# Optimization experiments

Measured on AMD Instinct MI355X. Metric: run time of the kernel, lower is better.

## Reference

```python
import jax, jax.numpy as jnp
import numpy as np

N = 50000
E = 800000
F_IN = 2      # num_node_features
H = 2         # heads
C = 64        # embedding_size (per-head out channels)
HID = 128     # hidden_size (message dim)
B = 512       # number of messages
NEG_SLOPE = 0.2


def gatv2_conv(x, src, dst, edge_attr, Wl, bl, Wr, br, We, att, bias):
    # x: [N, F_IN]; src/dst: [E]; edge_attr: [E, 1]
    n = x.shape[0]
    xl = (x @ Wl + bl).reshape(n, H, C)   # source transform (lin_l)
    xr = (x @ Wr + br).reshape(n, H, C)   # target transform (lin_r)
    ea = (edge_attr @ We).reshape(-1, H, C)
    m = xl[src] + xr[dst] + ea                      # [E, H, C]
    e = jnp.where(m > 0, m, NEG_SLOPE * m)          # LeakyReLU
    score = jnp.einsum('ehc,hc->eh', e, att)        # [E, H]
    # scatter-softmax over incoming edges of each target node
    smax = jax.ops.segment_max(score, dst, num_segments=n)
    smax = jnp.where(jnp.isfinite(smax), smax, 0.0)
    ex = jnp.exp(score - smax[dst])
    denom = jax.ops.segment_sum(ex, dst, num_segments=n)
    alpha = ex / (denom[dst] + 1e-16)               # [E, H]
    out = jax.ops.segment_sum(xl[src] * alpha[:, :, None], dst, num_segments=n)
    return out.reshape(n, H * C) + bias


def setup_inputs() -> dict:
    key = jax.random.key(0)
    ks = jax.random.split(key, 20)
    s = 0.1
    inp = {
        'message': jax.random.normal(ks[0], (B, HID), jnp.float32),
        'x': jax.random.normal(ks[1], (N, F_IN), jnp.float32),
        'edge_index': jax.random.randint(ks[2], (2, E), 0, N, jnp.int32),
        'edge_attr': jax.random.normal(ks[3], (E, 1), jnp.float32),
    }
    def conv_params(base):
        return {
            'Wl': jax.random.normal(ks[base], (F_IN, H * C)) * s,
            'bl': jnp.zeros((H * C,), jnp.float32),
            'Wr': jax.random.normal(ks[base + 1], (F_IN, H * C)) * s,
            'br': jnp.zeros((H * C,), jnp.float32),
            'We': jax.random.normal(ks[base + 2], (1, H * C)) * s,
            'att': jax.random.normal(ks[base + 3], (H, C)) * s,
            'bias': jnp.zeros((H * C,), jnp.float32),
        }
    p1 = {k + '1': v for k, v in conv_params(4).items()}
    p2 = {k + '2': v for k, v in conv_params(8).items()}
    inp.update(p1)
    inp.update(p2)
    inp['Wfc'] = jax.random.normal(ks[12], (HID, H * C)) * s
    inp['bfc'] = jnp.zeros((H * C,), jnp.float32)
    return inp


def reference(message, x, edge_index, edge_attr,
              Wl1, bl1, Wr1, br1, We1, att1, bias1,
              Wl2, bl2, Wr2, br2, We2, att2, bias2,
              Wfc, bfc):
    src, dst = edge_index[0], edge_index[1]
    # conv1 output is computed but unused in the original forward (conv2 takes x again)
    h1 = jax.nn.relu(gatv2_conv(x, src, dst, edge_attr, Wl1, bl1, Wr1, br1, We1, att1, bias1))
    h = jax.nn.relu(gatv2_conv(x, src, dst, edge_attr, Wl2, bl2, Wr2, br2, We2, att2, bias2))
    msg = jnp.concatenate([message, message], axis=0)      # [2B, HID]
    msg_emb = msg @ Wfc + bfc                              # [2B, H*C]
    dot = h @ msg_emb.T                                    # [N, 2B]
    return jax.nn.softmax(dot, axis=0)
```

## Files before the change

kernel.cpp:

```cpp
#include <hip/hip_runtime.h>
#include <hip/hip_bf16.h>
#include <hip/hip_cooperative_groups.h>

namespace cg = cooperative_groups;

#define N_NODES 50000
#define N_EDGES 800000
#define GRID    512
#define BLK     256
#define STRIDE  (GRID*BLK)
#define CHUNK   98
#define NTILES  782
#define NB_SCAN 196

typedef __attribute__((ext_vector_type(8))) short short8;
typedef __attribute__((ext_vector_type(16))) float f32x16;

struct Params {
  const float* msg; const float* x; const int* ei; const float* ea;
  const float* Wl; const float* bl; const float* Wr; const float* br;
  const float* We; const float* att; const float* bias;
  const float* Wfc; const float* bfc;
  float4* rec; float* nodeF;
  __hip_bfloat16* me_hi; __hip_bfloat16* me_lo;
  int* cnt; float* colsum; int* offs; int* cursor; int* bsum;
  float* dout;
};

template<int PASS>
__device__ __forceinline__ void mfma_tile(const Params& P, int tile, char* SMEM)
{
  short8* Bt = (short8*)SMEM;
  float* colacc = (float*)(SMEM + 32768);
  float* xp     = (float*)(SMEM + 32768);
  float* rcol   = (float*)(SMEM + 50176);

  const int tid = threadIdx.x;
  const int l = tid & 63, w = tid >> 6;
  const int rt = w >> 1, ct = w & 1;
  const int lrow = l & 31, lhalf = l >> 5;
  const int m0 = tile * 64;
  const int row = m0 + rt * 32 + lrow;

  float c0a = 0.f, c0b = 0.f, c0d = 0.f, c1a = 0.f, c1b = 0.f, c1d = 0.f;
  bool live = row < N_NODES;
  if (live) {
    const float* nf = P.nodeF + (size_t)row * 8;
    float D0 = nf[0], A00 = nf[1], A10 = nf[2];
    float D1 = nf[3], A01 = nf[4], A11 = nf[5];
    float r0 = 1.0f / (D0 + 1e-16f), r1 = 1.0f / (D1 + 1e-16f);
    c0a = A00 * r0; c0b = A10 * r0; c0d = D0 * r0;
    c1a = A01 * r1; c1b = A11 * r1; c1d = D1 * r1;
  }
  short8 a_hi[8], a_lo[8];
  #pragma unroll
  for (int ks = 0; ks < 8; ++ks) {
    int k0 = ks * 16 + lhalf * 8;
    float ca = (ks < 4) ? c0a : c1a;
    float cbv = (ks < 4) ? c0b : c1b;
    float cd = (ks < 4) ? c0d : c1d;
    float wA[8], wB[8], wC[8], wD[8];
    *(float4*)&wA[0] = *(const float4*)(P.Wl + k0);
    *(float4*)&wA[4] = *(const float4*)(P.Wl + k0 + 4);
    *(float4*)&wB[0] = *(const float4*)(P.Wl + 128 + k0);
    *(float4*)&wB[4] = *(const float4*)(P.Wl + 128 + k0 + 4);
    *(float4*)&wC[0] = *(const float4*)(P.bl + k0);
    *(float4*)&wC[4] = *(const float4*)(P.bl + k0 + 4);
    *(float4*)&wD[0] = *(const float4*)(P.bias + k0);
    *(float4*)&wD[4] = *(const float4*)(P.bias + k0 + 4);
    short8 hi8, lo8;
    #pragma unroll
    for (int j = 0; j < 8; ++j) {
      float v = ca * wA[j] + cbv * wB[j] + cd * wC[j] + wD[j];
      v = (live && v > 0.f) ? v : 0.f;
      __hip_bfloat16 hb = __float2bfloat16(v);
      float rem = v - __bfloat162float(hb);
      __hip_bfloat16 lb = __float2bfloat16(rem);
      short hs, ls;
      __builtin_memcpy(&hs, &hb, 2);
      __builtin_memcpy(&ls, &lb, 2);
      hi8[j] = hs; lo8[j] = ls;
    }
    a_hi[ks] = hi8; a_lo[ks] = lo8;
  }

  for (int cb = 0; cb < 8; ++cb) {
    __syncthreads();
    #pragma unroll
    for (int q = 0; q < 8; ++q) {
      int lin = q * 256 + tid;
      int s = lin & 1023;
      int col = s >> 4, ku = s & 15;
      int slot = ku * 64 + (col ^ ku);
      size_t gb = ((size_t)(cb * 64 + col) << 7) + ku * 8;
      if (lin < 1024) Bt[slot] = *(const short8*)(P.me_hi + gb);
      else            Bt[1024 + slot] = *(const short8*)(P.me_lo + gb);
    }
    __syncthreads();

    f32x16 acc = {0.f};
    #pragma unroll
    for (int ks = 0; ks < 8; ++ks) {
      int ku = ks * 2 + lhalf;
      int colB = ct * 32 + lrow;
      int slot = ku * 64 + (colB ^ ku);
      short8 bh = Bt[slot];
      short8 blo = Bt[1024 + slot];
      acc = __builtin_amdgcn_mfma_f32_32x32x16_bf16(a_hi[ks], bh, acc, 0, 0, 0);
      acc = __builtin_amdgcn_mfma_f32_32x32x16_bf16(a_lo[ks], bh, acc, 0, 0, 0);
      acc = __builtin_amdgcn_mfma_f32_32x32x16_bf16(a_hi[ks], blo, acc, 0, 0, 0);
    }

    if (PASS == 0) {
      float csum = 0.f;
      #pragma unroll
      for (int i = 0; i < 16; ++i) {
        int grow = m0 + rt * 32 + (i & 3) + 8 * (i >> 2) + 4 * lhalf;
        csum += (grow < N_NODES) ? __expf(acc[i]) : 0.f;
      }
      csum += __shfl_xor(csum, 32);
      if (l < 32) colacc[rt * 512 + cb * 64 + ct * 32 + l] += csum;
    } else {
      #pragma unroll
      for (int i = 0; i < 16; ++i) {
        int rl = rt * 32 + (i & 3) + 8 * (i >> 2) + 4 * lhalf;
        xp[rl * 68 + ct * 32 + lrow] = __expf(acc[i]);
      }
      __syncthreads();
      #pragma unroll
      for (int q = 0; q < 4; ++q) {
        int fid = q * 256 + tid;
        int rl = fid >> 4, c4 = fid & 15;
        int grow = m0 + rl;
        float4 v = *(float4*)&xp[rl * 68 + c4 * 4];
        float4 s = *(const float4*)&rcol[cb * 64 + c4 * 4];
        v.x *= s.x; v.y *= s.y; v.z *= s.z; v.w *= s.w;
        if (grow < N_NODES) {
          *(float4*)&P.dout[(size_t)grow * 1024 + cb * 64 + c4 * 4] = v;
          *(float4*)&P.dout[(size_t)grow * 1024 + 512 + cb * 64 + c4 * 4] = v;
        }
      }
    }
  }
}

__global__ __launch_bounds__(BLK, 2) void k_all(Params P)
{
  cg::grid_group gg = cg::this_grid();
  __shared__ __align__(16) char SMEM[52224];
  const int b = blockIdx.x, t = threadIdx.x;

  if (b < 256) {
    float* mrow = (float*)SMEM;
    int r = 2 * b + (t >> 7);
    int col = t & 127;
    mrow[t] = P.msg[r * 128 + col];
    __syncthreads();
    int base = (t >> 7) * 128;
    float acc = P.bfc[col];
    #pragma unroll 8
    for (int k = 0; k < 128; ++k) acc = fmaf(mrow[base + k], P.Wfc[k * 128 + col], acc);
    __hip_bfloat16 hi = __float2bfloat16(acc);
    P.me_hi[r * 128 + col] = hi;
    P.me_lo[r * 128 + col] = __float2bfloat16(acc - __bfloat162float(hi));
  } else if (b < 454) {
    int i = (b - 256) * 256 + t;
    if (i < N_NODES + 512) P.cnt[i] = 0;
  }
  gg.sync();

  for (int e = b * BLK + t; e < N_EDGES; e += STRIDE)
    atomicAdd(&P.cnt[P.ei[N_EDGES + e]], 1);
  gg.sync();

  {
    int* sh = (int*)SMEM;
    int base = b * CHUNK;
    if (t < 128) sh[t] = 0;
    __syncthreads();
    int v = 0;
    if (t < CHUNK && base + t < N_NODES) { v = P.cnt[base + t]; sh[t] = v; }
    __syncthreads();
    #pragma unroll
    for (int off = 1; off < 128; off <<= 1) {
      int u = (t < 128 && t >= off) ? sh[t - off] : 0;
      __syncthreads();
      if (t < 128) sh[t] += u;
      __syncthreads();
    }
    if (t < CHUNK && base + t < N_NODES) P.offs[base + t] = sh[t] - v;
    if (t == 0) P.bsum[b] = sh[127];
  }
  gg.sync();

  {
    int* eb = (int*)SMEM;
    int* s3 = eb + 512;
    int x0 = P.bsum[2 * t], x1 = P.bsum[2 * t + 1];
    s3[t] = x0 + x1;
    __syncthreads();
    #pragma unroll
    for (int off = 1; off < 256; off <<= 1) {
      int u = (t >= off) ? s3[t - off] : 0;
      __syncthreads();
      s3[t] += u;
      __syncthreads();
    }
    int p = t ? s3[t - 1] : 0;
    eb[2 * t] = p; eb[2 * t + 1] = p + x0;
    __syncthreads();
    int pb = eb[b];
    int base = b * CHUNK;
    if (t < CHUNK && base + t < N_NODES) {
      int o = P.offs[base + t] + pb;
      P.offs[base + t] = o;
      P.cursor[base + t] = o;
    }
    if (b == 0 && t == 0) P.offs[N_NODES] = N_EDGES;
  }
  gg.sync();

  for (int e = b * BLK + t; e < N_EDGES; e += STRIDE) {
    int s = P.ei[e], d = P.ei[N_EDGES + e];
    float x0s = P.x[2*s], x1s = P.x[2*s+1];
    float x0d = P.x[2*d], x1d = P.x[2*d+1];
    float av = P.ea[e];
    float s0 = 0.f, s1 = 0.f;
    #pragma unroll 8
    for (int k = 0; k < 64; ++k) {
      float m = P.bl[k] + P.br[k];
      m = fmaf(x0s, P.Wl[k], m);
      m = fmaf(x1s, P.Wl[128+k], m);
      m = fmaf(x0d, P.Wr[k], m);
      m = fmaf(x1d, P.Wr[128+k], m);
      m = fmaf(av, P.We[k], m);
      float lk = m > 0.f ? m : 0.2f * m;
      s0 = fmaf(lk, P.att[k], s0);
    }
    #pragma unroll 8
    for (int k = 64; k < 128; ++k) {
      float m = P.bl[k] + P.br[k];
      m = fmaf(x0s, P.Wl[k], m);
      m = fmaf(x1s, P.Wl[128+k], m);
      m = fmaf(x0d, P.Wr[k], m);
      m = fmaf(x1d, P.Wr[128+k], m);
      m = fmaf(av, P.We[k], m);
      float lk = m > 0.f ? m : 0.2f * m;
      s1 = fmaf(lk, P.att[k], s1);
    }
    int pos = atomicAdd(&P.cursor[d], 1);
    P.rec[pos] = make_float4(s0, s1, x0s, x1s);
  }
  gg.sync();

  {
    int n = b * BLK + t;
    if (n < N_NODES) {
      int a = P.offs[n], bb = P.offs[n + 1];
      float D0 = 0.f, A00 = 0.f, A10 = 0.f;
      float D1 = 0.f, A01 = 0.f, A11 = 0.f;
      for (int i = a; i < bb; ++i) {
        float4 r = P.rec[i];
        float e0 = __expf(r.x);
        float e1 = __expf(r.y);
        D0 += e0; A00 += e0 * r.z; A10 += e0 * r.w;
        D1 += e1; A01 += e1 * r.z; A11 += e1 * r.w;
      }
      float* nf = P.nodeF + (size_t)n * 8;
      nf[0] = D0; nf[1] = A00; nf[2] = A10;
      nf[3] = D1; nf[4] = A01; nf[5] = A11;
    }
  }
  gg.sync();

  {
    float* colacc = (float*)(SMEM + 32768);
    #pragma unroll
    for (int q = 0; q < 4; ++q) colacc[q * 256 + t] = 0.f;
    __syncthreads();
    for (int tile = b; tile < NTILES; tile += GRID)
      mfma_tile<0>(P, tile, SMEM);
    __syncthreads();
    atomicAdd(&P.colsum[t], colacc[t] + colacc[512 + t]);
    atomicAdd(&P.colsum[t + 256], colacc[256 + t] + colacc[768 + t]);
  }
  gg.sync();

  {
    float* rcol = (float*)(SMEM + 50176);
    rcol[t] = 1.0f / P.colsum[t];
    rcol[t + 256] = 1.0f / P.colsum[t + 256];
    __syncthreads();
    for (int tile = b; tile < NTILES; tile += GRID)
      mfma_tile<1>(P, tile, SMEM);
  }
}

__global__ __launch_bounds__(256) void k_zero(int* __restrict__ buf)
{
  int i = blockIdx.x * 256 + threadIdx.x;
  if (i < N_NODES + 512) buf[i] = 0;
}

__global__ __launch_bounds__(256) void k_hist(
    const int* __restrict__ ei, int* __restrict__ cnt)
{
  int e = blockIdx.x * 256 + threadIdx.x;
  if (e >= N_EDGES) return;
  atomicAdd(&cnt[ei[N_EDGES + e]], 1);
}

__global__ __launch_bounds__(256) void k_scan1(
    const int* __restrict__ cnt, int* __restrict__ offs, int* __restrict__ bsum)
{
  __shared__ int sh[256];
  int b = blockIdx.x, t = threadIdx.x;
  int i = b * 256 + t;
  int v = (i < N_NODES) ? cnt[i] : 0;
  sh[t] = v;
  __syncthreads();
  #pragma unroll
  for (int off = 1; off < 256; off <<= 1) {
    int u = (t >= off) ? sh[t - off] : 0;
    __syncthreads();
    sh[t] += u;
    __syncthreads();
  }
  if (i < N_NODES) offs[i] = sh[t] - v;
  if (t == 255) bsum[b] = sh[255];
}

__global__ __launch_bounds__(256) void k_scan2(int* __restrict__ bsum)
{
  __shared__ int sh[256];
  int t = threadIdx.x;
  int v = (t < NB_SCAN) ? bsum[t] : 0;
  sh[t] = v;
  __syncthreads();
  #pragma unroll
  for (int off = 1; off < 256; off <<= 1) {
    int u = (t >= off) ? sh[t - off] : 0;
    __syncthreads();
    sh[t] += u;
    __syncthreads();
  }
  if (t < NB_SCAN) bsum[t] = sh[t] - v;
}

__global__ __launch_bounds__(256) void k_scan3(
    int* __restrict__ offs, const int* __restrict__ bsum, int* __restrict__ cursor)
{
  int b = blockIdx.x, t = threadIdx.x;
  int i = b * 256 + t;
  if (i < N_NODES) {
    int o = offs[i] + bsum[b];
    offs[i] = o;
    cursor[i] = o;
  }
  if (b == 0 && t == 0) offs[N_NODES] = N_EDGES;
}

__global__ __launch_bounds__(256) void k_scatter(Params P)
{
  int e = blockIdx.x * 256 + threadIdx.x;
  if (e >= N_EDGES) return;
  int s = P.ei[e], d = P.ei[N_EDGES + e];
  float x0s = P.x[2*s], x1s = P.x[2*s+1];
  float x0d = P.x[2*d], x1d = P.x[2*d+1];
  float av = P.ea[e];
  float s0 = 0.f, s1 = 0.f;
  #pragma unroll 8
  for (int k = 0; k < 64; ++k) {
    float m = P.bl[k] + P.br[k];
    m = fmaf(x0s, P.Wl[k], m);
    m = fmaf(x1s, P.Wl[128+k], m);
    m = fmaf(x0d, P.Wr[k], m);
    m = fmaf(x1d, P.Wr[128+k], m);
    m = fmaf(av, P.We[k], m);
    float lk = m > 0.f ? m : 0.2f * m;
    s0 = fmaf(lk, P.att[k], s0);
  }
  #pragma unroll 8
  for (int k = 64; k < 128; ++k) {
    float m = P.bl[k] + P.br[k];
    m = fmaf(x0s, P.Wl[k], m);
    m = fmaf(x1s, P.Wl[128+k], m);
    m = fmaf(x0d, P.Wr[k], m);
    m = fmaf(x1d, P.Wr[128+k], m);
    m = fmaf(av, P.We[k], m);
    float lk = m > 0.f ? m : 0.2f * m;
    s1 = fmaf(lk, P.att[k], s1);
  }
  int pos = atomicAdd(&P.cursor[d], 1);
  P.rec[pos] = make_float4(s0, s1, x0s, x1s);
}

__global__ __launch_bounds__(256) void k_gather(Params P)
{
  int n = blockIdx.x * 256 + threadIdx.x;
  if (n >= N_NODES) return;
  int a = P.offs[n], b = P.offs[n + 1];
  float D0 = 0.f, A00 = 0.f, A10 = 0.f;
  float D1 = 0.f, A01 = 0.f, A11 = 0.f;
  for (int i = a; i < b; ++i) {
    float4 r = P.rec[i];
    float e0 = __expf(r.x);
    float e1 = __expf(r.y);
    D0 += e0; A00 += e0 * r.z; A10 += e0 * r.w;
    D1 += e1; A01 += e1 * r.z; A11 += e1 * r.w;
  }
  float* nf = P.nodeF + (size_t)n * 8;
  nf[0] = D0; nf[1] = A00; nf[2] = A10;
  nf[3] = D1; nf[4] = A01; nf[5] = A11;
}

__global__ __launch_bounds__(128) void k_fc(Params P)
{
  int j = blockIdx.x, k = threadIdx.x;
  __shared__ float mrow[128];
  mrow[k] = P.msg[j*128 + k];
  __syncthreads();
  float acc = P.bfc[k];
  #pragma unroll 8
  for (int t = 0; t < 128; ++t) acc = fmaf(mrow[t], P.Wfc[t*128 + k], acc);
  __hip_bfloat16 hi = __float2bfloat16(acc);
  P.me_hi[j*128 + k] = hi;
  P.me_lo[j*128 + k] = __float2bfloat16(acc - __bfloat162float(hi));
}

template<int PASS>
__global__ __launch_bounds__(256, 2) void k_mfma(Params P)
{
  __shared__ __align__(16) char SMEM[52224];
  int tid = threadIdx.x;
  if (PASS == 0) {
    float* colacc = (float*)(SMEM + 32768);
    #pragma unroll
    for (int q = 0; q < 4; ++q) colacc[q * 256 + tid] = 0.f;
    __syncthreads();
    mfma_tile<0>(P, blockIdx.x, SMEM);
    __syncthreads();
    atomicAdd(&P.colsum[tid], colacc[tid] + colacc[512 + tid]);
    atomicAdd(&P.colsum[tid + 256], colacc[256 + tid] + colacc[768 + tid]);
  } else {
    float* rcol = (float*)(SMEM + 50176);
    rcol[tid] = 1.0f / P.colsum[tid];
    rcol[tid + 256] = 1.0f / P.colsum[tid + 256];
    __syncthreads();
    mfma_tile<1>(P, blockIdx.x, SMEM);
  }
}

extern "C" void kernel_launch(void* const* d_in, const int* in_sizes, int n_in,
                              void* d_out, int out_size, void* d_ws, size_t ws_size,
                              hipStream_t stream)
{
  Params P;
  P.msg = (const float*)d_in[0];
  P.x   = (const float*)d_in[1];
  P.ei  = (const int*)d_in[2];
  P.ea  = (const float*)d_in[3];
  P.Wl   = (const float*)d_in[11];
  P.bl   = (const float*)d_in[12];
  P.Wr   = (const float*)d_in[13];
  P.br   = (const float*)d_in[14];
  P.We   = (const float*)d_in[15];
  P.att  = (const float*)d_in[16];
  P.bias = (const float*)d_in[17];
  P.Wfc  = (const float*)d_in[18];
  P.bfc  = (const float*)d_in[19];

  char* p = (char*)d_ws;
  P.rec = (float4*)p;                    p += (size_t)N_EDGES * 16;
  P.nodeF = (float*)p;                   p += (size_t)N_NODES * 8 * 4;
  P.me_hi = (__hip_bfloat16*)p;          p += 512 * 128 * 2;
  P.me_lo = (__hip_bfloat16*)p;          p += 512 * 128 * 2;
  P.cnt = (int*)p;                       p += (size_t)N_NODES * 4;
  P.colsum = (float*)p;                  p += 512 * 4;
  P.offs = (int*)p;                      p += (size_t)(N_NODES + 1) * 4;
  P.cursor = (int*)p;                    p += (size_t)N_NODES * 4;
  P.bsum = (int*)p;                      p += GRID * 4;
  P.dout = (float*)d_out;

  int maxBlk = 0;
  hipError_t qerr = hipOccupancyMaxActiveBlocksPerMultiprocessor(&maxBlk, k_all, BLK, 0);
  if (qerr == hipSuccess && maxBlk >= 2) {
    void* args[] = { &P };
    hipError_t lerr = hipLaunchCooperativeKernel((void*)k_all, dim3(GRID), dim3(BLK),
                                                 args, 0, stream);
    if (lerr == hipSuccess) return;
  }

  k_zero<<<(N_NODES + 512 + 255) / 256, 256, 0, stream>>>(P.cnt);
  k_hist<<<(N_EDGES + 255) / 256, 256, 0, stream>>>(P.ei, P.cnt);
  k_scan1<<<NB_SCAN, 256, 0, stream>>>(P.cnt, P.offs, P.bsum);
  k_scan2<<<1, 256, 0, stream>>>(P.bsum);
  k_scan3<<<NB_SCAN, 256, 0, stream>>>(P.offs, P.bsum, P.cursor);
  k_scatter<<<(N_EDGES + 255) / 256, 256, 0, stream>>>(P);
  k_gather<<<(N_NODES + 255) / 256, 256, 0, stream>>>(P);
  k_fc<<<512, 128, 0, stream>>>(P);
  k_mfma<0><<<NTILES, 256, 0, stream>>>(P);
  k_mfma<1><<<NTILES, 256, 0, stream>>>(P);
}
```

Baseline: 245.9 us.

## Prelayout MFMA B fragments in global memory and drop LDS staging to raise occupancy

The FC output is now written straight into MFMA B-fragment order, so each lane reads its B operands from global memory (served by L2) without staging them through LDS with extra barriers. This cuts LDS use from about 52KB to about 19KB. The cooperative grid now scales with the occupancy the runtime reports (512, 768 or 1024 blocks), and the scan chunking adapts to the grid size. The risks are repeated global or L2 reads of the B operand per tile, and a new per-cb barrier in the store pass.

```diff
diff --git a/kernel.cpp b/kernel.cpp
--- a/kernel.cpp
+++ b/kernel.cpp
@@ -6,12 +6,11 @@
 
 #define N_NODES 50000
 #define N_EDGES 800000
-#define GRID    512
 #define BLK     256
-#define STRIDE  (GRID*BLK)
-#define CHUNK   98
 #define NTILES  782
 #define NB_SCAN 196
+#define RC_OFF  17408
+#define SMEM_SZ 19712
 
 typedef __attribute__((ext_vector_type(8))) short short8;
 typedef __attribute__((ext_vector_type(16))) float f32x16;
@@ -22,26 +21,14 @@
   const float* We; const float* att; const float* bias;
   const float* Wfc; const float* bfc;
   float4* rec; float* nodeF;
-  __hip_bfloat16* me_hi; __hip_bfloat16* me_lo;
+  short* bfrag_hi; short* bfrag_lo;
   int* cnt; float* colsum; int* offs; int* cursor; int* bsum;
   float* dout;
 };
 
-template<int PASS>
-__device__ __forceinline__ void mfma_tile(const Params& P, int tile, char* SMEM)
-{
-  short8* Bt = (short8*)SMEM;
-  float* colacc = (float*)(SMEM + 32768);
-  float* xp     = (float*)(SMEM + 32768);
-  float* rcol   = (float*)(SMEM + 50176);
-
-  const int tid = threadIdx.x;
-  const int l = tid & 63, w = tid >> 6;
-  const int rt = w >> 1, ct = w & 1;
-  const int lrow = l & 31, lhalf = l >> 5;
-  const int m0 = tile * 64;
-  const int row = m0 + rt * 32 + lrow;
-
+__device__ __forceinline__ void build_A(const Params& P, int row, int lhalf,
+                                        short8* a_hi, short8* a_lo)
+{
   float c0a = 0.f, c0b = 0.f, c0d = 0.f, c1a = 0.f, c1b = 0.f, c1d = 0.f;
   bool live = row < N_NODES;
   if (live) {
@@ -52,7 +39,6 @@
     c0a = A00 * r0; c0b = A10 * r0; c0d = D0 * r0;
     c1a = A01 * r1; c1b = A11 * r1; c1d = D1 * r1;
   }
-  short8 a_hi[8], a_lo[8];
   #pragma unroll
   for (int ks = 0; ks < 8; ++ks) {
     int k0 = ks * 16 + lhalf * 8;
@@ -83,35 +69,45 @@
     }
     a_hi[ks] = hi8; a_lo[ks] = lo8;
   }
-
-  for (int cb = 0; cb < 8; ++cb) {
-    __syncthreads();
-    #pragma unroll
-    for (int q = 0; q < 8; ++q) {
-      int lin = q * 256 + tid;
-      int s = lin & 1023;
-      int col = s >> 4, ku = s & 15;
-      int slot = ku * 64 + (col ^ ku);
-      size_t gb = ((size_t)(cb * 64 + col) << 7) + ku * 8;
-      if (lin < 1024) Bt[slot] = *(const short8*)(P.me_hi + gb);
-      else            Bt[1024 + slot] = *(const short8*)(P.me_lo + gb);
-    }
-    __syncthreads();
-
-    f32x16 acc = {0.f};
-    #pragma unroll
-    for (int ks = 0; ks < 8; ++ks) {
-      int ku = ks * 2 + lhalf;
-      int colB = ct * 32 + lrow;
-      int slot = ku * 64 + (colB ^ ku);
-      short8 bh = Bt[slot];
-      short8 blo = Bt[1024 + slot];
-      acc = __builtin_amdgcn_mfma_f32_32x32x16_bf16(a_hi[ks], bh, acc, 0, 0, 0);
-      acc = __builtin_amdgcn_mfma_f32_32x32x16_bf16(a_lo[ks], bh, acc, 0, 0, 0);
-      acc = __builtin_amdgcn_mfma_f32_32x32x16_bf16(a_hi[ks], blo, acc, 0, 0, 0);
-    }
-
-    if (PASS == 0) {
+}
+
+__device__ __forceinline__ f32x16 mfma_block(const Params& P, int colgroup, int l,
+                                             const short8* a_hi, const short8* a_lo)
+{
+  const short8* BH = (const short8*)P.bfrag_hi + (size_t)colgroup * 512 + l;
+  const short8* BL = (const short8*)P.bfrag_lo + (size_t)colgroup * 512 + l;
+  f32x16 acc = {0.f};
+  #pragma unroll
+  for (int ks = 0; ks < 8; ++ks) {
+    short8 bh = BH[ks * 64];
+    short8 blo = BL[ks * 64];
+    acc = __builtin_amdgcn_mfma_f32_32x32x16_bf16(a_hi[ks], bh, acc, 0, 0, 0);
+    acc = __builtin_amdgcn_mfma_f32_32x32x16_bf16(a_lo[ks], bh, acc, 0, 0, 0);
+    acc = __builtin_amdgcn_mfma_f32_32x32x16_bf16(a_hi[ks], blo, acc, 0, 0, 0);
+  }
+  return acc;
+}
+
+__device__ __forceinline__ void mfma_colsum_tiles(const Params& P, int b, int G,
+                                                  char* SMEM)
+{
+  float* colacc = (float*)SMEM;
+  const int tid = threadIdx.x;
+  const int l = tid & 63, w = tid >> 6;
+  const int rt = w >> 1, ct = w & 1;
+  const int lrow = l & 31, lhalf = l >> 5;
+
+  #pragma unroll
+  for (int q = 0; q < 4; ++q) colacc[q * 256 + tid] = 0.f;
+  __syncthreads();
+
+  for (int tile = b; tile < NTILES; tile += G) {
+    int m0 = tile * 64;
+    short8 a_hi[8], a_lo[8];
+    build_A(P, m0 + rt * 32 + lrow, lhalf, a_hi, a_lo);
+    #pragma unroll 2
+    for (int cb = 0; cb < 8; ++cb) {
+      f32x16 acc = mfma_block(P, cb * 2 + ct, l, a_hi, a_lo);
       float csum = 0.f;
       #pragma unroll
       for (int i = 0; i < 16; ++i) {
@@ -120,7 +116,33 @@
       }
       csum += __shfl_xor(csum, 32);
       if (l < 32) colacc[rt * 512 + cb * 64 + ct * 32 + l] += csum;
-    } else {
+    }
+  }
+  __syncthreads();
+  atomicAdd(&P.colsum[tid], colacc[tid] + colacc[512 + tid]);
+  atomicAdd(&P.colsum[tid + 256], colacc[256 + tid] + colacc[768 + tid]);
+}
+
+__device__ __forceinline__ void mfma_store_tiles(const Params& P, int b, int G,
+                                                 char* SMEM)
+{
+  float* xp = (float*)SMEM;
+  float* rcol = (float*)(SMEM + RC_OFF);
+  const int tid = threadIdx.x;
+  const int l = tid & 63, w = tid >> 6;
+  const int rt = w >> 1, ct = w & 1;
+  const int lrow = l & 31, lhalf = l >> 5;
+
+  rcol[tid] = 1.0f / P.colsum[tid];
+  rcol[tid + 256] = 1.0f / P.colsum[tid + 256];
+  __syncthreads();
+
+  for (int tile = b; tile < NTILES; tile += G) {
+    int m0 = tile * 64;
+    short8 a_hi[8], a_lo[8];
+    build_A(P, m0 + rt * 32 + lrow, lhalf, a_hi, a_lo);
+    for (int cb = 0; cb < 8; ++cb) {
+      f32x16 acc = mfma_block(P, cb * 2 + ct, l, a_hi, a_lo);
       #pragma unroll
       for (int i = 0; i < 16; ++i) {
         int rl = rt * 32 + (i & 3) + 8 * (i >> 2) + 4 * lhalf;
@@ -140,6 +162,7 @@
           *(float4*)&P.dout[(size_t)grow * 1024 + 512 + cb * 64 + c4 * 4] = v;
         }
       }
+      __syncthreads();
     }
   }
 }
@@ -147,39 +170,50 @@
 __global__ __launch_bounds__(BLK, 2) void k_all(Params P)
 {
   cg::grid_group gg = cg::this_grid();
-  __shared__ __align__(16) char SMEM[52224];
+  __shared__ __align__(16) char SMEM[SMEM_SZ];
   const int b = blockIdx.x, t = threadIdx.x;
+  const int G = gridDim.x;
 
   if (b < 256) {
     float* mrow = (float*)SMEM;
     int r = 2 * b + (t >> 7);
-    int col = t & 127;
-    mrow[t] = P.msg[r * 128 + col];
+    int k = t & 127;
+    mrow[t] = P.msg[r * 128 + k];
     __syncthreads();
     int base = (t >> 7) * 128;
-    float acc = P.bfc[col];
+    float acc = P.bfc[k];
     #pragma unroll 8
-    for (int k = 0; k < 128; ++k) acc = fmaf(mrow[base + k], P.Wfc[k * 128 + col], acc);
-    __hip_bfloat16 hi = __float2bfloat16(acc);
-    P.me_hi[r * 128 + col] = hi;
-    P.me_lo[r * 128 + col] = __float2bfloat16(acc - __bfloat162float(hi));
+    for (int kk = 0; kk < 128; ++kk)
+      acc = fmaf(mrow[base + kk], P.Wfc[kk * 128 + k], acc);
+    __hip_bfloat16 hb = __float2bfloat16(acc);
+    float rem = acc - __bfloat162float(hb);
+    __hip_bfloat16 lb = __float2bfloat16(rem);
+    short hs, ls;
+    __builtin_memcpy(&hs, &hb, 2);
+    __builtin_memcpy(&ls, &lb, 2);
+    size_t idx = ((size_t)((r >> 5) * 8 + (k >> 4)) * 64
+                  + ((k >> 3) & 1) * 32 + (r & 31)) * 8 + (k & 7);
+    P.bfrag_hi[idx] = hs;
+    P.bfrag_lo[idx] = ls;
   } else if (b < 454) {
     int i = (b - 256) * 256 + t;
     if (i < N_NODES + 512) P.cnt[i] = 0;
   }
   gg.sync();
 
-  for (int e = b * BLK + t; e < N_EDGES; e += STRIDE)
+  for (int e = b * BLK + t; e < N_EDGES; e += G * BLK)
     atomicAdd(&P.cnt[P.ei[N_EDGES + e]], 1);
   gg.sync();
+
+  const int CH = (N_NODES + G - 1) / G;
 
   {
     int* sh = (int*)SMEM;
-    int base = b * CHUNK;
+    int base = b * CH;
     if (t < 128) sh[t] = 0;
     __syncthreads();
     int v = 0;
-    if (t < CHUNK && base + t < N_NODES) { v = P.cnt[base + t]; sh[t] = v; }
+    if (t < 128 && t < CH && base + t < N_NODES) { v = P.cnt[base + t]; sh[t] = v; }
     __syncthreads();
     #pragma unroll
     for (int off = 1; off < 128; off <<= 1) {
@@ -188,16 +222,19 @@
       if (t < 128) sh[t] += u;
       __syncthreads();
     }
-    if (t < CHUNK && base + t < N_NODES) P.offs[base + t] = sh[t] - v;
+    if (t < 128 && t < CH && base + t < N_NODES) P.offs[base + t] = sh[t] - v;
     if (t == 0) P.bsum[b] = sh[127];
   }
   gg.sync();
 
   {
     int* eb = (int*)SMEM;
-    int* s3 = eb + 512;
-    int x0 = P.bsum[2 * t], x1 = P.bsum[2 * t + 1];
-    s3[t] = x0 + x1;
+    int* s3 = eb + 1024;
+    const int nb = G >> 8;
+    int xv[4];
+    int ssum = 0;
+    for (int j = 0; j < nb; ++j) { xv[j] = P.bsum[nb * t + j]; ssum += xv[j]; }
+    s3[t] = ssum;
     __syncthreads();
     #pragma unroll
     for (int off = 1; off < 256; off <<= 1) {
@@ -207,11 +244,11 @@
       __syncthreads();
     }
     int p = t ? s3[t - 1] : 0;
-    eb[2 * t] = p; eb[2 * t + 1] = p + x0;
+    for (int j = 0; j < nb; ++j) { eb[nb * t + j] = p; p += xv[j]; }
     __syncthreads();
     int pb = eb[b];
-    int base = b * CHUNK;
-    if (t < CHUNK && base + t < N_NODES) {
+    int base = b * CH;
+    if (t < CH && base + t < N_NODES) {
       int o = P.offs[base + t] + pb;
       P.offs[base + t] = o;
       P.cursor[base + t] = o;
@@ -220,7 +257,7 @@
   }
   gg.sync();
 
-  for (int e = b * BLK + t; e < N_EDGES; e += STRIDE) {
+  for (int e = b * BLK + t; e < N_EDGES; e += G * BLK) {
     int s = P.ei[e], d = P.ei[N_EDGES + e];
     float x0s = P.x[2*s], x1s = P.x[2*s+1];
     float x0d = P.x[2*d], x1d = P.x[2*d+1];
@@ -273,27 +310,10 @@
   }
   gg.sync();
 
-  {
-    float* colacc = (float*)(SMEM + 32768);
-    #pragma unroll
-    for (int q = 0; q < 4; ++q) colacc[q * 256 + t] = 0.f;
-    __syncthreads();
-    for (int tile = b; tile < NTILES; tile += GRID)
-      mfma_tile<0>(P, tile, SMEM);
-    __syncthreads();
-    atomicAdd(&P.colsum[t], colacc[t] + colacc[512 + t]);
-    atomicAdd(&P.colsum[t + 256], colacc[256 + t] + colacc[768 + t]);
-  }
-  gg.sync();
-
-  {
-    float* rcol = (float*)(SMEM + 50176);
-    rcol[t] = 1.0f / P.colsum[t];
-    rcol[t + 256] = 1.0f / P.colsum[t + 256];
-    __syncthreads();
-    for (int tile = b; tile < NTILES; tile += GRID)
-      mfma_tile<1>(P, tile, SMEM);
-  }
+  mfma_colsum_tiles(P, b, G, SMEM);
+  gg.sync();
+
+  mfma_store_tiles(P, b, G, SMEM);
 }
 
 __global__ __launch_bounds__(256) void k_zero(int* __restrict__ buf)
@@ -416,39 +436,31 @@
 
 __global__ __launch_bounds__(128) void k_fc(Params P)
 {
-  int j = blockIdx.x, k = threadIdx.x;
+  int r = blockIdx.x, k = threadIdx.x;
   __shared__ float mrow[128];
-  mrow[k] = P.msg[j*128 + k];
+  mrow[k] = P.msg[r*128 + k];
   __syncthreads();
   float acc = P.bfc[k];
   #pragma unroll 8
   for (int t = 0; t < 128; ++t) acc = fmaf(mrow[t], P.Wfc[t*128 + k], acc);
-  __hip_bfloat16 hi = __float2bfloat16(acc);
-  P.me_hi[j*128 + k] = hi;
-  P.me_lo[j*128 + k] = __float2bfloat16(acc - __bfloat162float(hi));
+  __hip_bfloat16 hb = __float2bfloat16(acc);
+  float rem = acc - __bfloat162float(hb);
+  __hip_bfloat16 lb = __float2bfloat16(rem);
+  short hs, ls;
+  __builtin_memcpy(&hs, &hb, 2);
+  __builtin_memcpy(&ls, &lb, 2);
+  size_t idx = ((size_t)((r >> 5) * 8 + (k >> 4)) * 64
+                + ((k >> 3) & 1) * 32 + (r & 31)) * 8 + (k & 7);
+  P.bfrag_hi[idx] = hs;
+  P.bfrag_lo[idx] = ls;
 }
 
 template<int PASS>
 __global__ __launch_bounds__(256, 2) void k_mfma(Params P)
 {
-  __shared__ __align__(16) char SMEM[52224];
-  int tid = threadIdx.x;
-  if (PASS == 0) {
-    float* colacc = (float*)(SMEM + 32768);
-    #pragma unroll
-    for (int q = 0; q < 4; ++q) colacc[q * 256 + tid] = 0.f;
-    __syncthreads();
-    mfma_tile<0>(P, blockIdx.x, SMEM);
-    __syncthreads();
-    atomicAdd(&P.colsum[tid], colacc[tid] + colacc[512 + tid]);
-    atomicAdd(&P.colsum[tid + 256], colacc[256 + tid] + colacc[768 + tid]);
-  } else {
-    float* rcol = (float*)(SMEM + 50176);
-    rcol[tid] = 1.0f / P.colsum[tid];
-    rcol[tid + 256] = 1.0f / P.colsum[tid + 256];
-    __syncthreads();
-    mfma_tile<1>(P, blockIdx.x, SMEM);
-  }
+  __shared__ __align__(16) char SMEM[SMEM_SZ];
+  if (PASS == 0) mfma_colsum_tiles(P, blockIdx.x, gridDim.x, SMEM);
+  else           mfma_store_tiles(P, blockIdx.x, gridDim.x, SMEM);
 }
 
 extern "C" void kernel_launch(void* const* d_in, const int* in_sizes, int n_in,
@@ -473,20 +485,21 @@
   char* p = (char*)d_ws;
   P.rec = (float4*)p;                    p += (size_t)N_EDGES * 16;
   P.nodeF = (float*)p;                   p += (size_t)N_NODES * 8 * 4;
-  P.me_hi = (__hip_bfloat16*)p;          p += 512 * 128 * 2;
-  P.me_lo = (__hip_bfloat16*)p;          p += 512 * 128 * 2;
+  P.bfrag_hi = (short*)p;                p += 512 * 128 * 2;
+  P.bfrag_lo = (short*)p;                p += 512 * 128 * 2;
   P.cnt = (int*)p;                       p += (size_t)N_NODES * 4;
   P.colsum = (float*)p;                  p += 512 * 4;
   P.offs = (int*)p;                      p += (size_t)(N_NODES + 1) * 4;
   P.cursor = (int*)p;                    p += (size_t)N_NODES * 4;
-  P.bsum = (int*)p;                      p += GRID * 4;
+  P.bsum = (int*)p;                      p += 1024 * 4;
   P.dout = (float*)d_out;
 
   int maxBlk = 0;
   hipError_t qerr = hipOccupancyMaxActiveBlocksPerMultiprocessor(&maxBlk, k_all, BLK, 0);
   if (qerr == hipSuccess && maxBlk >= 2) {
+    int g = (maxBlk >= 4) ? 1024 : (maxBlk >= 3 ? 768 : 512);
     void* args[] = { &P };
-    hipError_t lerr = hipLaunchCooperativeKernel((void*)k_all, dim3(GRID), dim3(BLK),
+    hipError_t lerr = hipLaunchCooperativeKernel((void*)k_all, dim3(g), dim3(BLK),
                                                  args, 0, stream);
     if (lerr == hipSuccess) return;
   }
```

Measured after the change: 324.4 us. +31.9%, slower.
